# Kernel tuning notes

Measured on AMD Instinct MI355X. Metric: run time of the kernel, lower is better.

## Reference

```python
import jax, jax.numpy as jnp
import numpy as np

D = 4
R = 6
P = 2 * R + 1          # 13, fine match window
N = P * P              # 169
MR = 12
MP = 2 * MR + 1        # 25, coarse search window
DIL_INT = 15


def corr_sampler(t, r, Pp, dil):
    """SpatialCorrelationSampler(kernel_size=1, patch_size=Pp, dilation_patch=dil).
    t, r: (b,c,h,w). Returns (b,Pp,Pp,h,w): corr[b,p,q,y,x] = sum_c t[b,c,y,x]*r[b,c,y+dil*(p-R),x+dil*(q-R)] (zero pad)."""
    Rr = (Pp - 1) // 2
    pad = Rr * dil
    b, c, h, w = t.shape
    rp = jnp.pad(r, ((0, 0), (0, 0), (pad, pad), (pad, pad)))
    d = (jnp.arange(Pp) - Rr) * dil
    yi = jnp.arange(h)[None, :] + d[:, None] + pad      # (Pp,h)
    xi = jnp.arange(w)[None, :] + d[:, None] + pad      # (Pp,w)
    g = rp[:, :, yi[:, None, :, None], xi[None, :, None, :]]  # (b,c,Pp,Pp,h,w)
    return jnp.einsum('bchw,bcpqhw->bpqhw', t, g)


def bilinear_patch(src, py, px):
    """deform_im2col: bilinear-sample a PxP patch around (x+off_x+dx, y+off_y+dy).
    src (b,c,h,w); py (b,P,1,h,w); px (b,1,P,h,w) float coords. Returns (b,c,P,P,h,w)."""
    b, c, h, w = src.shape
    y0 = jnp.floor(py); x0 = jnp.floor(px)
    wy = py - y0; wx = px - x0
    y0 = y0.astype(jnp.int32); x0 = x0.astype(jnp.int32)

    def corner(yi, xi, wgt):
        valid = (yi >= 0) & (yi < h) & (xi >= 0) & (xi < w)
        yc = jnp.clip(yi, 0, h - 1)
        xc = jnp.clip(xi, 0, w - 1)
        v = jax.vmap(lambda im, a, bb: im[:, a, bb])(src, yc, xc)  # (b,c,P,P,h,w)
        return v * (wgt * valid)[:, None]

    out = corner(y0, x0, (1 - wy) * (1 - wx))
    out = out + corner(y0, x0 + 1, (1 - wy) * wx)
    out = out + corner(y0 + 1, x0, wy * (1 - wx))
    out = out + corner(y0 + 1, x0 + 1, wy * wx)
    return out


def unfold_patches(src, Pp):
    """F.unfold(src, kernel_size=Pp, padding=Rr) -> (b,c,Pp,Pp,h,w)."""
    Rr = (Pp - 1) // 2
    b, c, h, w = src.shape
    sp = jnp.pad(src, ((0, 0), (0, 0), (Rr, Rr), (Rr, Rr)))
    yi = jnp.arange(h)[None, :] + jnp.arange(Pp)[:, None]
    xi = jnp.arange(w)[None, :] + jnp.arange(Pp)[:, None]
    return sp[:, :, yi[:, None, :, None], xi[None, :, None, :]]


def _forward(feats_r, feats_t, quantized_r, nsearch, dirates):
    nref = feats_r.shape[0]
    b, c, h, w = feats_t.shape
    f32 = feats_t.dtype
    dy = (jnp.arange(P) - R).astype(f32)
    gy, gx = jnp.meshgrid(jnp.arange(-MR, MR + 1).astype(f32),
                          jnp.arange(-MR, MR + 1).astype(f32), indexing='ij')
    corrs = []
    py = px = None
    for si in range(nsearch):
        d = dirates[si]
        cc = corr_sampler(feats_t, feats_r[si], MP, d)                     # (b,MP,MP,h,w)
        cc = jax.nn.softmax(cc.reshape(b, MP * MP, h * w), axis=1).reshape(b, MP, MP, h, w)
        off_x = jnp.einsum('bpqhw,pq->bhw', cc, gx) * d                    # soft-argmax offsets
        off_y = jnp.einsum('bpqhw,pq->bhw', cc, gy) * d
        # sample coords: (b,P,1,h,w) / (b,1,P,h,w)
        py = (off_y + jnp.arange(h).astype(f32)[None, :, None])[:, None, None] + dy[:, None, None, None]
        px = (off_x + jnp.arange(w).astype(f32)[None, None, :])[:, None, None] + dy[None, :, None, None]
        col = bilinear_patch(feats_r[si], py, px)                          # (b,c,P,P,h,w)
        corrs.append(jnp.einsum('bchw,bcpqhw->bpqhw', feats_t, col).reshape(b, N, h * w))
    for ind in range(nsearch, nref):
        corrs.append(corr_sampler(feats_t, feats_r[ind], P, 1).reshape(b, N, h * w))
    corr = jax.nn.softmax(jnp.concatenate(corrs, 1), axis=1)               # (b,nref*N,hw)
    qr = quantized_r[:, :, :, ::D, ::D]                                    # prep(): (nref,b,C,h,w)
    cols = []
    for i in range(nsearch):
        # NOTE: faithful to original -- uses offset0 from the LAST coarse-search iteration
        cols.append(bilinear_patch(qr[i], py, px).reshape(b, -1, N, h * w))
    for i in range(nsearch, nref):
        cols.append(unfold_patches(qr[i], P).reshape(b, -1, N, h * w))
    image_uf = jnp.concatenate(cols, 2)                                    # (b,C,nref*N,hw)
    out = jnp.einsum('bnx,bcnx->bcx', corr, image_uf)
    return out.reshape(b, qr.shape[2], h, w)


def reference(feats_r, feats_t, quantized_r, ref_index, current_ind):
    gaps = [int(current_ind) - int(x) for x in np.asarray(ref_index)]
    nsearch = sum(g > DIL_INT for g in gaps)
    dirates = [min(4, g // DIL_INT + 1) for g in gaps if g > DIL_INT]
    return _forward(feats_r, feats_t, quantized_r, nsearch, dirates)


def setup_inputs():
    key = jax.random.key(0)
    k1, k2, k3 = jax.random.split(key, 3)
    feats_r = jax.random.normal(k1, (3, 1, 64, 48, 84), jnp.float32)
    feats_t = jax.random.normal(k2, (1, 64, 48, 84), jnp.float32)
    quantized_r = jax.random.uniform(k3, (3, 1, 32, 192, 336), jnp.float32)
    return dict(feats_r=feats_r, feats_t=feats_t, quantized_r=quantized_r,
                ref_index=np.arange(3), current_ind=16)
```

## Files before the change

### kernel.cpp

```cpp
#include <hip/hip_runtime.h>
#include <math.h>

constexpr int H  = 48;
constexpr int W  = 84;
constexpr int HW = H * W;
constexpr int C  = 64;
constexpr int CQ = 32;
constexpr int QH = 192;
constexpr int QW = 336;
constexpr int NREF = 3;

typedef short bf16x8 __attribute__((ext_vector_type(8)));
typedef float f32x4  __attribute__((ext_vector_type(4)));

#define DEV __device__ __forceinline__

DEV unsigned short f2bf_rn(float f) {
  unsigned int u = __builtin_bit_cast(unsigned int, f);
  u += 0x7FFFu + ((u >> 16) & 1u);
  return (unsigned short)(u >> 16);
}
DEV float bf2f(unsigned short h) {
  unsigned int u = ((unsigned int)h) << 16;
  return __builtin_bit_cast(float, u);
}

DEV float block_sum(float v, float* red) {
  __syncthreads();
#pragma unroll
  for (int o = 32; o > 0; o >>= 1) v += __shfl_down(v, o, 64);
  if ((threadIdx.x & 63) == 0) red[threadIdx.x >> 6] = v;
  __syncthreads();
  return red[0] + red[1] + red[2] + red[3];
}
DEV float block_max(float v, float* red) {
  __syncthreads();
#pragma unroll
  for (int o = 32; o > 0; o >>= 1) v = fmaxf(v, __shfl_down(v, o, 64));
  if ((threadIdx.x & 63) == 0) red[threadIdx.x >> 6] = v;
  __syncthreads();
  return fmaxf(fmaxf(red[0], red[1]), fmaxf(red[2], red[3]));
}

__global__ __launch_bounds__(256) void k_prep(const float* __restrict__ fr,
                                              const float* __restrict__ ft,
                                              const float* __restrict__ q,
                                              float* __restrict__ frT,
                                              float* __restrict__ ftT,
                                              unsigned short* __restrict__ rbh,
                                              unsigned short* __restrict__ rbl,
                                              unsigned short* __restrict__ tbh,
                                              unsigned short* __restrict__ tbl,
                                              unsigned short* __restrict__ qrb,
                                              float* __restrict__ accum) {
  const int mode = blockIdx.y;
  const int tid = threadIdx.x;

  if (mode < 4) {
    __shared__ float lds[64][65];
    const int r = mode;
    const float* src = (r < NREF) ? (fr + (size_t)r * C * HW) : ft;
    float* dstF          = (r < NREF) ? (frT + (size_t)r * HW * C) : ftT;
    unsigned short* dstH = (r < NREF) ? (rbh + (size_t)r * HW * C) : tbh;
    unsigned short* dstL = (r < NREF) ? (rbl + (size_t)r * HW * C) : tbl;
    const int pb = blockIdx.x * 64;
    const int a = tid & 63, b = tid >> 6;
#pragma unroll
    for (int i = 0; i < 16; i++) {
      int c = i * 4 + b;
      lds[c][a] = src[c * HW + pb + a];
    }
    __syncthreads();
#pragma unroll
    for (int i = 0; i < 16; i++) {
      int p = i * 4 + b;
      float v = lds[a][p];
      int o = (pb + p) * C + a;
      dstF[o] = v;
      unsigned short h = f2bf_rn(v);
      dstH[o] = h;
      dstL[o] = f2bf_rn(v - bf2f(h));
    }
  } else if (mode < 7) {
    const int k = mode - 4;
#pragma unroll
    for (int i = 0; i < 8; i++) {
      const int o = blockIdx.x * 2048 + i * 256 + tid;
      const int pix = o >> 5, c = o & 31;
      const int yq = pix / W, xq = pix - yq * W;
      const float v = q[(size_t)((k * CQ + c) * QH + yq * 4) * QW + xq * 4];
      qrb[(size_t)k * HW * CQ + o] = f2bf_rn(v);
    }
  } else {
    const int nacc = NREF * HW * 3;
    for (int i = blockIdx.x * 256 + tid; i < nacc; i += 63 * 256) accum[i] = 0.f;
  }
}

DEV f32x4 band_mfma(bf16x8 ah0, bf16x8 ah1, bf16x8 al0, bf16x8 al1,
                    const unsigned short* __restrict__ rH,
                    const unsigned short* __restrict__ rL,
                    int bpix, int fko, bool bv) {
  const bf16x8 zf = {0, 0, 0, 0, 0, 0, 0, 0};
  bf16x8 bh0 = *reinterpret_cast<const bf16x8*>(rH + (size_t)bpix * C + fko);
  bf16x8 bh1 = *reinterpret_cast<const bf16x8*>(rH + (size_t)bpix * C + fko + 32);
  bf16x8 bl0 = *reinterpret_cast<const bf16x8*>(rL + (size_t)bpix * C + fko);
  bf16x8 bl1 = *reinterpret_cast<const bf16x8*>(rL + (size_t)bpix * C + fko + 32);
  if (!bv) { bh0 = zf; bh1 = zf; bl0 = zf; bl1 = zf; }
  f32x4 acc = {0.f, 0.f, 0.f, 0.f};
  acc = __builtin_amdgcn_mfma_f32_16x16x32_bf16(ah0, bh0, acc, 0, 0, 0);
  acc = __builtin_amdgcn_mfma_f32_16x16x32_bf16(ah1, bh1, acc, 0, 0, 0);
  acc = __builtin_amdgcn_mfma_f32_16x16x32_bf16(ah0, bl0, acc, 0, 0, 0);
  acc = __builtin_amdgcn_mfma_f32_16x16x32_bf16(ah1, bl1, acc, 0, 0, 0);
  acc = __builtin_amdgcn_mfma_f32_16x16x32_bf16(al0, bh0, acc, 0, 0, 0);
  acc = __builtin_amdgcn_mfma_f32_16x16x32_bf16(al1, bh1, acc, 0, 0, 0);
  return acc;
}

__global__ __launch_bounds__(256) void k_mfma(
    const unsigned short* __restrict__ rbh, const unsigned short* __restrict__ rbl,
    const unsigned short* __restrict__ tbh, const unsigned short* __restrict__ tbl,
    const int* __restrict__ ridx, const int* __restrict__ curp,
    float* __restrict__ accum, float* __restrict__ lg) {
  const int si = blockIdx.z / 7, pz = blockIdx.z % 7;
  const int gap = curp[0] - ridx[si];
  const bool isSearch = gap > 15;
  const int lane = threadIdx.x & 63, wave = threadIdx.x >> 6;
  const int sub = pz * 4 + wave;
  if (isSearch) { if (sub >= 25) return; }
  else          { if (sub >= 13) return; }

  const int y = blockIdx.y, x0 = blockIdx.x * 16;
  const int fpx = lane & 15, fko = (lane >> 4) * 8;

  const bool pValid = (x0 + fpx) < W;
  const int apix = pValid ? (y * W + x0 + fpx) : 0;
  const bf16x8 zf = {0, 0, 0, 0, 0, 0, 0, 0};
  bf16x8 ah0 = *reinterpret_cast<const bf16x8*>(tbh + (size_t)apix * C + fko);
  bf16x8 ah1 = *reinterpret_cast<const bf16x8*>(tbh + (size_t)apix * C + fko + 32);
  bf16x8 al0 = *reinterpret_cast<const bf16x8*>(tbl + (size_t)apix * C + fko);
  bf16x8 al1 = *reinterpret_cast<const bf16x8*>(tbl + (size_t)apix * C + fko + 32);
  if (!pValid) { ah0 = zf; ah1 = zf; al0 = zf; al1 = zf; }

  const unsigned short* rH = rbh + (size_t)si * HW * C;
  const unsigned short* rL = rbl + (size_t)si * HW * C;

  if (isSearch) {
    int d = gap / 15 + 1; if (d > 4) d = 4;
    const int Zoff = (d == 1) ? 16 : (d == 2) ? 32 : 48;
    const int NZT  = (d == 1) ? 3  : (d == 2) ? 5  : 7;
    const int Minv = (d == 1) ? 65536 : (d == 2) ? 32768 : (d == 3) ? 21846 : 16384;
    const int p = sub;
    const int row2 = y + d * (p - 12);
    const bool rv = (row2 >= 0) && (row2 < H);

    float se[4] = {0.f, 0.f, 0.f, 0.f};
    float sq[4] = {0.f, 0.f, 0.f, 0.f};
    for (int zt = 0; zt < NZT; ++zt) {
      const int z0 = x0 - Zoff + zt * 16;
      const int z = z0 + fpx;
      const bool bv = rv && (z >= 0) && (z < W);
      const int bpix = bv ? (row2 * W + z) : 0;
      f32x4 acc = band_mfma(ah0, ah1, al0, al1, rH, rL, bpix, fko, bv);
#pragma unroll
      for (int r = 0; r < 4; r++) {
        const int xl = (lane >> 4) * 4 + r;
        const int qnum = (z0 + fpx) - (x0 + xl) + 12 * d;
        if (qnum >= 0) {
          const int qq = (qnum * Minv) >> 16;
          if (qq * d == qnum && qq < 25) {
            const float e = __expf(fminf(acc[r], 60.f));
            se[r] += e;
            sq[r] += e * (float)(qq - 12);
          }
        }
      }
    }
#pragma unroll
    for (int r = 0; r < 4; r++) {
#pragma unroll
      for (int o = 1; o < 16; o <<= 1) {
        se[r] += __shfl_xor(se[r], o, 64);
        sq[r] += __shfl_xor(sq[r], o, 64);
      }
    }
    if (fpx == 0) {
#pragma unroll
      for (int r = 0; r < 4; r++) {
        const int xl = (lane >> 4) * 4 + r;
        if (x0 + xl < W) {
          float* a = accum + (size_t)(si * HW + y * W + x0 + xl) * 3;
          atomicAdd(a + 0, se[r]);
          atomicAdd(a + 1, se[r] * (float)(p - 12));
          atomicAdd(a + 2, sq[r]);
        }
      }
    }
  } else {
    const int dp = sub;
    const int row2 = y + dp - 6;
    const bool rv = (row2 >= 0) && (row2 < H);
    for (int zt = 0; zt < 3; ++zt) {
      const int z0 = x0 - 16 + zt * 16;
      const int z = z0 + fpx;
      const bool bv = rv && (z >= 0) && (z < W);
      const int bpix = bv ? (row2 * W + z) : 0;
      f32x4 acc = band_mfma(ah0, ah1, al0, al1, rH, rL, bpix, fko, bv);
#pragma unroll
      for (int r = 0; r < 4; r++) {
        const int xl = (lane >> 4) * 4 + r;
        const int qq = (z0 + fpx) - (x0 + xl) + 6;
        if (qq >= 0 && qq < 13 && (x0 + xl) < W)
          lg[(size_t)(y * W + x0 + xl) * 512 + si * 169 + dp * 13 + qq] = acc[r];
      }
    }
  }
}

__global__ __launch_bounds__(256) void k_pix(
    const float* __restrict__ frT, const float* __restrict__ ftT,
    const unsigned short* __restrict__ qrb, const float* __restrict__ lg,
    const float* __restrict__ accum,
    const int* __restrict__ ridx, const int* __restrict__ curp,
    float* __restrict__ out) {
  const int pix = blockIdx.x;
  const int y = pix / W, x = pix - y * W;
  const int tid = threadIdx.x;
  const int lane = tid & 63, wave = tid >> 6;

  __shared__ __align__(16) float tl[64];
  __shared__ float C14[14][16];
  __shared__ float sP[4];
  __shared__ float sLs[4];
  __shared__ float lgs[512];
  __shared__ float red[4];
  __shared__ int   wloc[640];
  __shared__ float wval[640];
  __shared__ float part[4][32];

  const int cur = curp[0];
  bool srch[NREF];
  int dd[NREF];
  int ls = -1;
#pragma unroll
  for (int k = 0; k < NREF; k++) {
    const int g = cur - ridx[k];
    srch[k] = (g > 15);
    int d = g / 15 + 1;
    dd[k] = d > 4 ? 4 : d;
    if (srch[k]) ls = k;
  }

  if (tid < 64) tl[tid] = ftT[(size_t)pix * C + tid];
  __syncthreads();

  for (int si = 0; si < NREF; ++si) {
    if (!srch[si]) continue;
    if (tid == 0) {
      const float* a = accum + (size_t)(si * HW + pix) * 3;
      const float inv = 1.f / a[0];
      const float oy = (float)dd[si] * a[1] * inv, ox = (float)dd[si] * a[2] * inv;
      const float fy = (float)y + oy, fx = (float)x + ox;
      const float Y0 = floorf(fy), X0 = floorf(fx);
      sP[0] = Y0; sP[1] = X0; sP[2] = fy - Y0; sP[3] = fx - X0;
      if (si == ls) { sLs[0] = Y0; sLs[1] = X0; sLs[2] = fy - Y0; sLs[3] = fx - X0; }
    }
    __syncthreads();
    const int iY = (int)sP[0], iX = (int)sP[1];
    const float wy = sP[2], wx = sP[3];
    const float* frB = frT + (size_t)si * HW * C;

    if (tid < 224) {
      const int j = tid >> 4, cg = tid & 15;
      const int col = iX - 6 + j;
      const bool cv = (col >= 0) && (col < W);
      const float4 tv = *reinterpret_cast<const float4*>(&tl[cg * 4]);
#pragma unroll 2
      for (int i = 0; i < 14; ++i) {
        const int row = iY - 6 + i;
        float s = 0.f;
        if (cv && row >= 0 && row < H) {
          const float4 rv4 = *reinterpret_cast<const float4*>(
              frB + (size_t)(row * W + col) * C + cg * 4);
          s = tv.x * rv4.x + tv.y * rv4.y + tv.z * rv4.z + tv.w * rv4.w;
        }
        s += __shfl_xor(s, 1, 64);
        s += __shfl_xor(s, 2, 64);
        s += __shfl_xor(s, 4, 64);
        s += __shfl_xor(s, 8, 64);
        if (cg == 0) C14[i][j] = s;
      }
    }
    __syncthreads();
    for (int it = tid; it < 169; it += 256) {
      const int i = it / 13, j = it - i * 13;
      lgs[si * 169 + it] =
          (1.f - wy) * ((1.f - wx) * C14[i][j] + wx * C14[i][j + 1]) +
          wy * ((1.f - wx) * C14[i + 1][j] + wx * C14[i + 1][j + 1]);
    }
    __syncthreads();
  }

  for (int k = 0; k < NREF; k++) {
    if (srch[k]) continue;
    for (int it = tid; it < 169; it += 256)
      lgs[k * 169 + it] = lg[(size_t)pix * 512 + k * 169 + it];
  }
  __syncthreads();

  float m = -1e30f;
  for (int i = tid; i < 507; i += 256) m = fmaxf(m, lgs[i]);
  m = block_max(m, red);
  float se = 0.f;
  for (int i = tid; i < 507; i += 256) {
    const float e = __expf(lgs[i] - m);
    lgs[i] = e;
    se += e;
  }
  se = block_sum(se, red);
  const float inv = 1.f / se;

  int bases[NREF], tot = 0;
#pragma unroll
  for (int k = 0; k < NREF; k++) { bases[k] = tot; tot += srch[k] ? 196 : 169; }
  const int NT = (tot + 63) >> 6;

  int liY = 0, liX = 0; float lwy = 0.f, lwx = 0.f;
  if (ls >= 0) { liY = (int)sLs[0]; liX = (int)sLs[1]; lwy = sLs[2]; lwx = sLs[3]; }

  for (int k = 0; k < NREF; k++) {
    const int base = bases[k];
    if (srch[k]) {
      const float* wk = &lgs[k * 169];
      for (int it = tid; it < 196; it += 256) {
        const int i = it / 14, j = it - i * 14;
        const float a00 = (i < 13 && j < 13) ? wk[i * 13 + j] : 0.f;
        const float a01 = (i < 13 && j >= 1) ? wk[i * 13 + j - 1] : 0.f;
        const float a10 = (i >= 1 && j < 13) ? wk[(i - 1) * 13 + j] : 0.f;
        const float a11 = (i >= 1 && j >= 1) ? wk[(i - 1) * 13 + j - 1] : 0.f;
        const float wv = (1.f - lwy) * ((1.f - lwx) * a00 + lwx * a01) +
                         lwy * ((1.f - lwx) * a10 + lwx * a11);
        const int row = liY + i - 6, col = liX + j - 6;
        const bool v = (unsigned)row < (unsigned)H && (unsigned)col < (unsigned)W;
        wloc[base + it] = v ? (k * HW + row * W + col) : 0;
        wval[base + it] = v ? wv : 0.f;
      }
    } else {
      for (int it = tid; it < 169; it += 256) {
        const int p = it / 13, q = it - p * 13;
        const int row = y + p - 6, col = x + q - 6;
        const bool v = (unsigned)row < (unsigned)H && (unsigned)col < (unsigned)W;
        wloc[base + it] = v ? (k * HW + row * W + col) : 0;
        wval[base + it] = v ? lgs[k * 169 + it] : 0.f;
      }
    }
  }
  for (int e = tot + tid; e < NT * 64; e += 256) { wloc[e] = 0; wval[e] = 0.f; }
  __syncthreads();

  const int c4 = lane & 3, l16 = lane >> 2;
  float a[8] = {0.f, 0.f, 0.f, 0.f, 0.f, 0.f, 0.f, 0.f};
  for (int t = 0; t < NT; ++t) {
    const int e = t * 64 + wave * 16 + l16;
    const float wv = wval[e];
    const int loc = wloc[e];
    const bf16x8 qv = *reinterpret_cast<const bf16x8*>(
        qrb + (size_t)loc * CQ + c4 * 8);
#pragma unroll
    for (int j = 0; j < 8; j++)
      a[j] = fmaf(wv, bf2f((unsigned short)qv[j]), a[j]);
  }
#pragma unroll
  for (int o = 4; o < 64; o <<= 1) {
#pragma unroll
    for (int j = 0; j < 8; j++) a[j] += __shfl_xor(a[j], o, 64);
  }
  if (l16 == 0) {
#pragma unroll
    for (int j = 0; j < 8; j++) part[wave][c4 * 8 + j] = a[j];
  }
  __syncthreads();
  if (tid < 32) {
    const float s = part[0][tid] + part[1][tid] + part[2][tid] + part[3][tid];
    out[(size_t)tid * HW + pix] = s * inv;
  }
}

extern "C" void kernel_launch(void* const* d_in, const int* in_sizes, int n_in,
                              void* d_out, int out_size, void* d_ws, size_t ws_size,
                              hipStream_t stream) {
  (void)in_sizes; (void)n_in; (void)out_size; (void)ws_size;
  const float* fr = (const float*)d_in[0];
  const float* ft = (const float*)d_in[1];
  const float* q  = (const float*)d_in[2];
  const int* ridx = (const int*)d_in[3];
  const int* cur  = (const int*)d_in[4];
  float* out = (float*)d_out;

  char* ws = (char*)d_ws;
  float* frT  = (float*)ws;                   ws += (size_t)NREF * HW * C * 4;
  float* ftT  = (float*)ws;                   ws += (size_t)HW * C * 4;
  unsigned short* rbh = (unsigned short*)ws;  ws += (size_t)NREF * HW * C * 2;
  unsigned short* rbl = (unsigned short*)ws;  ws += (size_t)NREF * HW * C * 2;
  unsigned short* tbh = (unsigned short*)ws;  ws += (size_t)HW * C * 2;
  unsigned short* tbl = (unsigned short*)ws;  ws += (size_t)HW * C * 2;
  unsigned short* qrb = (unsigned short*)ws;  ws += (size_t)NREF * HW * CQ * 2;
  float* lg    = (float*)ws;                  ws += (size_t)HW * 512 * 4;
  float* accum = (float*)ws;                  ws += (size_t)NREF * HW * 3 * 4;

  k_prep<<<dim3(HW / 64, 8), dim3(256), 0, stream>>>(fr, ft, q, frT, ftT,
                                                     rbh, rbl, tbh, tbl, qrb, accum);
  k_mfma<<<dim3(6, H, NREF * 7), dim3(256), 0, stream>>>(rbh, rbl, tbh, tbl,
                                                         ridx, cur, accum, lg);
  k_pix<<<dim3(HW), dim3(256), 0, stream>>>(frT, ftT, qrb, lg, accum,
                                            ridx, cur, out);
}
```

Before: 81.86 us.

## Pair two band rows per wave in MFMA kernel and vectorize logit layout

```diff
diff --git a/kernel.cpp b/kernel.cpp
--- a/kernel.cpp
+++ b/kernel.cpp
@@ -9,6 +9,8 @@
 constexpr int QH = 192;
 constexpr int QW = 336;
 constexpr int NREF = 3;
+constexpr int SLG = 176;
+constexpr int LGS = 544;
 
 typedef short bf16x8 __attribute__((ext_vector_type(8)));
 typedef float f32x4  __attribute__((ext_vector_type(4)));
@@ -53,11 +55,11 @@
                                               unsigned short* __restrict__ tbl,
                                               unsigned short* __restrict__ qrb,
                                               float* __restrict__ accum) {
+  __shared__ float lds[64][65];
   const int mode = blockIdx.y;
   const int tid = threadIdx.x;
 
   if (mode < 4) {
-    __shared__ float lds[64][65];
     const int r = mode;
     const float* src = (r < NREF) ? (fr + (size_t)r * C * HW) : ft;
     float* dstF          = (r < NREF) ? (frT + (size_t)r * HW * C) : ftT;
@@ -83,14 +85,22 @@
     }
   } else if (mode < 7) {
     const int k = mode - 4;
-#pragma unroll
-    for (int i = 0; i < 8; i++) {
-      const int o = blockIdx.x * 2048 + i * 256 + tid;
-      const int pix = o >> 5, c = o & 31;
-      const int yq = pix / W, xq = pix - yq * W;
-      const float v = q[(size_t)((k * CQ + c) * QH + yq * 4) * QW + xq * 4];
-      qrb[(size_t)k * HW * CQ + o] = f2bf_rn(v);
-    }
+    const int yq = blockIdx.x;
+    if (yq >= H) return;
+    unsigned short* qs = (unsigned short*)lds;
+    const int c = tid >> 3, xo = tid & 7;
+#pragma unroll
+    for (int i = 0; i < 11; i++) {
+      const int x = xo + 8 * i;
+      if (x < W) {
+        const float v = q[((size_t)(k * CQ + c) * QH + yq * 4) * QW + x * 4];
+        qs[x * CQ + c] = f2bf_rn(v);
+      }
+    }
+    __syncthreads();
+    const unsigned int* qsu = (const unsigned int*)qs;
+    unsigned int* dst = (unsigned int*)(qrb + (size_t)k * HW * CQ + (size_t)yq * W * CQ);
+    for (int o = tid; o < W * CQ / 2; o += 256) dst[o] = qsu[o];
   } else {
     const int nacc = NREF * HW * 3;
     for (int i = blockIdx.x * 256 + tid; i < nacc; i += 63 * 256) accum[i] = 0.f;
@@ -122,17 +132,23 @@
     const unsigned short* __restrict__ tbh, const unsigned short* __restrict__ tbl,
     const int* __restrict__ ridx, const int* __restrict__ curp,
     float* __restrict__ accum, float* __restrict__ lg) {
-  const int si = blockIdx.z / 7, pz = blockIdx.z % 7;
+  const int bid = blockIdx.x;
+  const int idx = bid >> 3;
+  const int ychunk = bid & 7;
+  const int yloc = idx / 72;
+  const int rest = idx - yloc * 72;
+  const int zi = rest / 6;
+  const int x0i = rest - zi * 6;
+  const int y = ychunk * 6 + yloc;
+  const int x0 = x0i * 16;
+  const int si = zi >> 2, pz = zi & 3;
+
   const int gap = curp[0] - ridx[si];
   const bool isSearch = gap > 15;
   const int lane = threadIdx.x & 63, wave = threadIdx.x >> 6;
-  const int sub = pz * 4 + wave;
-  if (isSearch) { if (sub >= 25) return; }
-  else          { if (sub >= 13) return; }
-
-  const int y = blockIdx.y, x0 = blockIdx.x * 16;
+  if (!isSearch && pz >= 2) return;
+
   const int fpx = lane & 15, fko = (lane >> 4) * 8;
-
   const bool pValid = (x0 + fpx) < W;
   const int apix = pValid ? (y * W + x0 + fpx) : 0;
   const bf16x8 zf = {0, 0, 0, 0, 0, 0, 0, 0};
@@ -150,18 +166,27 @@
     const int Zoff = (d == 1) ? 16 : (d == 2) ? 32 : 48;
     const int NZT  = (d == 1) ? 3  : (d == 2) ? 5  : 7;
     const int Minv = (d == 1) ? 65536 : (d == 2) ? 32768 : (d == 3) ? 21846 : 16384;
-    const int p = sub;
-    const int row2 = y + d * (p - 12);
-    const bool rv = (row2 >= 0) && (row2 < H);
-
-    float se[4] = {0.f, 0.f, 0.f, 0.f};
-    float sq[4] = {0.f, 0.f, 0.f, 0.f};
+    const int slot = pz * 4 + wave;
+    const int p1 = slot, p2 = slot + 16;
+    const float w2 = (p2 <= 24) ? 1.f : 0.f;
+    const int row2a = y + d * (p1 - 12);
+    const int row2b = y + d * (p2 - 12);
+    const bool rva = (row2a >= 0) && (row2a < H);
+    const bool rvb = (w2 > 0.f) && (row2b >= 0) && (row2b < H);
+
+    float seA[4] = {0.f, 0.f, 0.f, 0.f};
+    float seB[4] = {0.f, 0.f, 0.f, 0.f};
+    float sq[4]  = {0.f, 0.f, 0.f, 0.f};
+
     for (int zt = 0; zt < NZT; ++zt) {
       const int z0 = x0 - Zoff + zt * 16;
       const int z = z0 + fpx;
-      const bool bv = rv && (z >= 0) && (z < W);
-      const int bpix = bv ? (row2 * W + z) : 0;
-      f32x4 acc = band_mfma(ah0, ah1, al0, al1, rH, rL, bpix, fko, bv);
+      const bool zv = (z >= 0) && (z < W);
+      const bool bva = rva && zv, bvb = rvb && zv;
+      const int bpa = bva ? (row2a * W + z) : 0;
+      const int bpb = bvb ? (row2b * W + z) : 0;
+      f32x4 accA = band_mfma(ah0, ah1, al0, al1, rH, rL, bpa, fko, bva);
+      f32x4 accB = band_mfma(ah0, ah1, al0, al1, rH, rL, bpb, fko, bvb);
 #pragma unroll
       for (int r = 0; r < 4; r++) {
         const int xl = (lane >> 4) * 4 + r;
@@ -169,9 +194,10 @@
         if (qnum >= 0) {
           const int qq = (qnum * Minv) >> 16;
           if (qq * d == qnum && qq < 25) {
-            const float e = __expf(fminf(acc[r], 60.f));
-            se[r] += e;
-            sq[r] += e * (float)(qq - 12);
+            const float eA = __expf(fminf(accA[r], 60.f));
+            const float eB = w2 * __expf(fminf(accB[r], 60.f));
+            seA[r] += eA; seB[r] += eB;
+            sq[r] += (eA + eB) * (float)(qq - 12);
           }
         }
       }
@@ -180,8 +206,9 @@
     for (int r = 0; r < 4; r++) {
 #pragma unroll
       for (int o = 1; o < 16; o <<= 1) {
-        se[r] += __shfl_xor(se[r], o, 64);
-        sq[r] += __shfl_xor(sq[r], o, 64);
+        seA[r] += __shfl_xor(seA[r], o, 64);
+        seB[r] += __shfl_xor(seB[r], o, 64);
+        sq[r]  += __shfl_xor(sq[r],  o, 64);
       }
     }
     if (fpx == 0) {
@@ -190,28 +217,39 @@
         const int xl = (lane >> 4) * 4 + r;
         if (x0 + xl < W) {
           float* a = accum + (size_t)(si * HW + y * W + x0 + xl) * 3;
-          atomicAdd(a + 0, se[r]);
-          atomicAdd(a + 1, se[r] * (float)(p - 12));
+          atomicAdd(a + 0, seA[r] + seB[r]);
+          atomicAdd(a + 1, seA[r] * (float)(p1 - 12) + seB[r] * (float)(p2 - 12));
           atomicAdd(a + 2, sq[r]);
         }
       }
     }
   } else {
-    const int dp = sub;
-    const int row2 = y + dp - 6;
-    const bool rv = (row2 >= 0) && (row2 < H);
+    const int slot = pz * 4 + wave;
+    const int dp1 = slot, dp2 = slot + 8;
+    const bool has2 = dp2 < 13;
+    const int row2a = y + dp1 - 6;
+    const int row2b = y + dp2 - 6;
+    const bool rva = (row2a >= 0) && (row2a < H);
+    const bool rvb = has2 && (row2b >= 0) && (row2b < H);
+
     for (int zt = 0; zt < 3; ++zt) {
       const int z0 = x0 - 16 + zt * 16;
       const int z = z0 + fpx;
-      const bool bv = rv && (z >= 0) && (z < W);
-      const int bpix = bv ? (row2 * W + z) : 0;
-      f32x4 acc = band_mfma(ah0, ah1, al0, al1, rH, rL, bpix, fko, bv);
+      const bool zv = (z >= 0) && (z < W);
+      const bool bva = rva && zv, bvb = rvb && zv;
+      const int bpa = bva ? (row2a * W + z) : 0;
+      const int bpb = bvb ? (row2b * W + z) : 0;
+      f32x4 accA = band_mfma(ah0, ah1, al0, al1, rH, rL, bpa, fko, bva);
+      f32x4 accB = band_mfma(ah0, ah1, al0, al1, rH, rL, bpb, fko, bvb);
 #pragma unroll
       for (int r = 0; r < 4; r++) {
         const int xl = (lane >> 4) * 4 + r;
         const int qq = (z0 + fpx) - (x0 + xl) + 6;
-        if (qq >= 0 && qq < 13 && (x0 + xl) < W)
-          lg[(size_t)(y * W + x0 + xl) * 512 + si * 169 + dp * 13 + qq] = acc[r];
+        if (qq >= 0 && qq < 13 && (x0 + xl) < W) {
+          float* lb = lg + (size_t)(y * W + x0 + xl) * LGS + si * SLG;
+          lb[dp1 * 13 + qq] = accA[r];
+          if (has2) lb[dp2 * 13 + qq] = accB[r];
+        }
       }
     }
   }
@@ -232,7 +270,7 @@
   __shared__ float C14[14][16];
   __shared__ float sP[4];
   __shared__ float sLs[4];
-  __shared__ float lgs[512];
+  __shared__ __align__(16) float lgs[3 * SLG];
   __shared__ float red[4];
   __shared__ int   wloc[640];
   __shared__ float wval[640];
@@ -252,6 +290,7 @@
   }
 
   if (tid < 64) tl[tid] = ftT[(size_t)pix * C + tid];
+  if (tid < 21) lgs[(tid / 7) * SLG + 169 + (tid % 7)] = -1e30f;
   __syncthreads();
 
   for (int si = 0; si < NREF; ++si) {
@@ -294,7 +333,7 @@
     __syncthreads();
     for (int it = tid; it < 169; it += 256) {
       const int i = it / 13, j = it - i * 13;
-      lgs[si * 169 + it] =
+      lgs[si * SLG + it] =
           (1.f - wy) * ((1.f - wx) * C14[i][j] + wx * C14[i][j + 1]) +
           wy * ((1.f - wx) * C14[i + 1][j] + wx * C14[i + 1][j + 1]);
     }
@@ -303,16 +342,20 @@
 
   for (int k = 0; k < NREF; k++) {
     if (srch[k]) continue;
-    for (int it = tid; it < 169; it += 256)
-      lgs[k * 169 + it] = lg[(size_t)pix * 512 + k * 169 + it];
+    const float* src = lg + (size_t)pix * LGS + k * SLG;
+    for (int it = tid; it < 42; it += 256)
+      *reinterpret_cast<float4*>(&lgs[k * SLG + it * 4]) =
+          *reinterpret_cast<const float4*>(src + it * 4);
+    if (tid == 42 * 4 - 168)
+      lgs[k * SLG + 168] = src[168];
   }
   __syncthreads();
 
   float m = -1e30f;
-  for (int i = tid; i < 507; i += 256) m = fmaxf(m, lgs[i]);
+  for (int i = tid; i < 3 * SLG; i += 256) m = fmaxf(m, lgs[i]);
   m = block_max(m, red);
   float se = 0.f;
-  for (int i = tid; i < 507; i += 256) {
+  for (int i = tid; i < 3 * SLG; i += 256) {
     const float e = __expf(lgs[i] - m);
     lgs[i] = e;
     se += e;
@@ -331,7 +374,7 @@
   for (int k = 0; k < NREF; k++) {
     const int base = bases[k];
     if (srch[k]) {
-      const float* wk = &lgs[k * 169];
+      const float* wk = &lgs[k * SLG];
       for (int it = tid; it < 196; it += 256) {
         const int i = it / 14, j = it - i * 14;
         const float a00 = (i < 13 && j < 13) ? wk[i * 13 + j] : 0.f;
@@ -351,7 +394,7 @@
         const int row = y + p - 6, col = x + q - 6;
         const bool v = (unsigned)row < (unsigned)H && (unsigned)col < (unsigned)W;
         wloc[base + it] = v ? (k * HW + row * W + col) : 0;
-        wval[base + it] = v ? lgs[k * 169 + it] : 0.f;
+        wval[base + it] = v ? lgs[k * SLG + it] : 0.f;
       }
     }
   }
@@ -405,13 +448,13 @@
   unsigned short* tbh = (unsigned short*)ws;  ws += (size_t)HW * C * 2;
   unsigned short* tbl = (unsigned short*)ws;  ws += (size_t)HW * C * 2;
   unsigned short* qrb = (unsigned short*)ws;  ws += (size_t)NREF * HW * CQ * 2;
-  float* lg    = (float*)ws;                  ws += (size_t)HW * 512 * 4;
+  float* lg    = (float*)ws;                  ws += (size_t)HW * LGS * 4;
   float* accum = (float*)ws;                  ws += (size_t)NREF * HW * 3 * 4;
 
   k_prep<<<dim3(HW / 64, 8), dim3(256), 0, stream>>>(fr, ft, q, frT, ftT,
                                                      rbh, rbl, tbh, tbl, qrb, accum);
-  k_mfma<<<dim3(6, H, NREF * 7), dim3(256), 0, stream>>>(rbh, rbl, tbh, tbl,
-                                                         ridx, cur, accum, lg);
+  k_mfma<<<dim3(8 * 432), dim3(256), 0, stream>>>(rbh, rbl, tbh, tbl,
+                                                  ridx, cur, accum, lg);
   k_pix<<<dim3(HW), dim3(256), 0, stream>>>(frT, ftT, qrb, lg, accum,
                                             ridx, cur, out);
 }
```

Result: slower. 86.96 us (+6.2%).
